# Kernel tuning notes

Hardware: AMD Instinct MI355X
Metric: run time of the kernel (lower is better)

Reference implementation:

```python
import jax, jax.numpy as jnp
import numpy as np

K = 512
U = 2
TEMP_BERN = 0.67
TEMP_CAT = 0.67
EULER = 0.5772156649015329
EPS = 1e-8
UEPS = 1e-6


def setup_inputs() -> dict:
    key = jax.random.key(0)
    ks = jax.random.split(key, 3)
    B, D = 16384, 1024
    inputs = jax.random.normal(ks[0], (B, D), jnp.float32)
    # glorot-normal-ish init for mW
    mW = jax.random.normal(ks[1], (D, K * U), jnp.float32) * jnp.sqrt(2.0 / (D + K * U))
    sW = jnp.full((D, K * U), -5.0, jnp.float32)
    conc1 = jnp.full((K,), 2.0, jnp.float32)
    conc0 = jnp.full((K,), 0.5453, jnp.float32)
    t_pi = jax.random.uniform(ks[2], (D, K), jnp.float32, 4.0, 5.0)
    biases = jnp.full((K * U,), 0.1, jnp.float32)
    return {"inputs": inputs, "mW": mW, "sW": sW, "conc1": conc1,
            "conc0": conc0, "t_pi": t_pi, "biases": biases}


def _uniform(k, shape):
    return jax.random.uniform(k, shape, jnp.float32, UEPS, 1.0 - UEPS)


def reference(inputs, mW, sW, conc1, conc0, t_pi, biases):
    rk = jax.random.split(jax.random.key(42), 4)

    # --- reparameterized weights W = mW + eps * softplus(sW) ---
    sW_sp = jax.nn.softplus(sW)
    eps = jax.lax.stop_gradient(jax.random.normal(rk[0], mW.shape, jnp.float32))
    W = mW + eps * sW_sp
    kl_weights = -0.5 * jnp.mean(2.0 * sW_sp - jnp.square(mW) - jnp.square(sW_sp) + 1.0)
    layer_loss = kl_weights / 60000.0

    # --- IBP: relaxed Bernoulli sample of t_pi ([D, K]) ---
    u = _uniform(rk[1], t_pi.shape)
    logistic = jnp.log(u) - jnp.log1p(-u)
    z_sample = jax.nn.sigmoid((t_pi + logistic) / TEMP_BERN)  # bin_concrete_sample
    z = jnp.tile(z_sample, (1, U))  # [D, K*U], column order u*K+k (as in TF code)

    # Kumaraswamy stick-breaking prior: cumprod along axis 0 (TF default)
    a_sp = jax.nn.softplus(conc1)  # [K]
    b_sp = jax.nn.softplus(conc0)  # [K]
    uk = _uniform(rk[2], t_pi.shape)
    q_u = jnp.power(1.0 - jnp.power(uk, 1.0 / b_sp), 1.0 / a_sp)  # kumaraswamy_sample
    prior_pi = jnp.cumprod(q_u, axis=0)
    q = jax.nn.sigmoid(t_pi)
    kl_z = jnp.sum(q * (jnp.log(q + EPS) - jnp.log(prior_pi + EPS)))

    # KL(Kumaraswamy(a,b) || Beta(1,1)); (beta-1) series term vanishes
    kl_sticks = jnp.sum(((a_sp - 1.0) / a_sp) * (-EULER - jax.scipy.special.digamma(b_sp) - 1.0 / b_sp)
                        + jnp.log(a_sp * b_sp + EPS) - (b_sp - 1.0) / b_sp)
    layer_loss = layer_loss + kl_sticks + kl_z

    W = z * W
    out = inputs @ W + biases  # [B, K*U]

    # --- LWTA activation via Gumbel-softmax over U competitors ---
    logits = out.reshape(-1, K, U)  # [B, K, U]
    g = -jnp.log(-jnp.log(_uniform(rk[3], logits.shape)))
    xi = jax.nn.softmax((logits + g) / TEMP_CAT, axis=-1)  # concrete_sample
    out_act = (logits * xi).reshape(out.shape)
    q_xi = jax.nn.softmax(logits, axis=-1)
    kl_xi = jnp.mean(jnp.sum(q_xi * (jnp.log(q_xi + EPS) - jnp.log(1.0 / U)), axis=1))
    layer_loss = layer_loss + kl_xi

    return out_act, layer_loss
```

## Files before the change

### kernel.cpp

```cpp
#include <hip/hip_runtime.h>
#include <stdint.h>
#include <math.h>

#define B_N   16384
#define D_N   1024
#define K_N   512
#define KU_N  1024
#define EPS_F 1e-8f
#define TEMP  0.67f
#define EULERC 0.5772156649015329f

#define HEPS  524288
#define HU    262144
#define HG    8388608

typedef uint32_t u32;
typedef __attribute__((ext_vector_type(4))) float f32x4;
typedef __attribute__((ext_vector_type(4))) unsigned int u32x4;
typedef __attribute__((ext_vector_type(8))) __bf16 bf16x8;

#define TF_ROT(x, r) (((x) << (r)) | ((x) >> (32 - (r))))

__host__ __device__ static inline void threefry2x32(u32 k0, u32 k1,
                                                    u32 x0, u32 x1,
                                                    u32* o0, u32* o1) {
  u32 ks2 = k0 ^ k1 ^ 0x1BD11BDAu;
  x0 += k0; x1 += k1;
  x0 += x1; x1 = TF_ROT(x1, 13); x1 ^= x0;
  x0 += x1; x1 = TF_ROT(x1, 15); x1 ^= x0;
  x0 += x1; x1 = TF_ROT(x1, 26); x1 ^= x0;
  x0 += x1; x1 = TF_ROT(x1, 6);  x1 ^= x0;
  x0 += k1; x1 += ks2 + 1u;
  x0 += x1; x1 = TF_ROT(x1, 17); x1 ^= x0;
  x0 += x1; x1 = TF_ROT(x1, 29); x1 ^= x0;
  x0 += x1; x1 = TF_ROT(x1, 16); x1 ^= x0;
  x0 += x1; x1 = TF_ROT(x1, 24); x1 ^= x0;
  x0 += ks2; x1 += k0 + 2u;
  x0 += x1; x1 = TF_ROT(x1, 13); x1 ^= x0;
  x0 += x1; x1 = TF_ROT(x1, 15); x1 ^= x0;
  x0 += x1; x1 = TF_ROT(x1, 26); x1 ^= x0;
  x0 += x1; x1 = TF_ROT(x1, 6);  x1 ^= x0;
  x0 += k0; x1 += k1 + 3u;
  x0 += x1; x1 = TF_ROT(x1, 17); x1 ^= x0;
  x0 += x1; x1 = TF_ROT(x1, 29); x1 ^= x0;
  x0 += x1; x1 = TF_ROT(x1, 16); x1 ^= x0;
  x0 += x1; x1 = TF_ROT(x1, 24); x1 ^= x0;
  x0 += k1; x1 += ks2 + 4u;
  x0 += x1; x1 = TF_ROT(x1, 13); x1 ^= x0;
  x0 += x1; x1 = TF_ROT(x1, 15); x1 ^= x0;
  x0 += x1; x1 = TF_ROT(x1, 26); x1 ^= x0;
  x0 += x1; x1 = TF_ROT(x1, 6);  x1 ^= x0;
  x0 += ks2; x1 += k0 + 5u;
  *o0 = x0; *o1 = x1;
}

__device__ static inline float bits_to_u01(u32 b) {
  u32 f = (b >> 9) | 0x3f800000u;
  return __uint_as_float(f) - 1.0f;
}
__device__ static inline float unif_f(u32 b, float lo, float hi) {
  float f = bits_to_u01(b);
  return fmaxf(lo, f * (hi - lo) + lo);
}
__device__ static inline float erfinv_f(float x) {
  float w = -log1pf(-x * x);
  float p;
  if (w < 5.f) {
    w -= 2.5f;
    p = 2.81022636e-08f;
    p = fmaf(p, w, 3.43273939e-07f);
    p = fmaf(p, w, -3.5233877e-06f);
    p = fmaf(p, w, -4.39150654e-06f);
    p = fmaf(p, w, 0.00021858087f);
    p = fmaf(p, w, -0.00125372503f);
    p = fmaf(p, w, -0.00417768164f);
    p = fmaf(p, w, 0.246640727f);
    p = fmaf(p, w, 1.50140941f);
  } else {
    w = sqrtf(w) - 3.f;
    p = -0.000200214257f;
    p = fmaf(p, w, 0.000100950558f);
    p = fmaf(p, w, 0.00134934322f);
    p = fmaf(p, w, -0.00367342844f);
    p = fmaf(p, w, 0.00573950773f);
    p = fmaf(p, w, -0.0076224613f);
    p = fmaf(p, w, 0.00943887047f);
    p = fmaf(p, w, 1.00167406f);
    p = fmaf(p, w, 2.83297682f);
  }
  return p * x;
}
__device__ static inline float softplus_f(float x) {
  return fmaxf(x, 0.f) + log1pf(expf(-fabsf(x)));
}
__device__ static inline float rcp_f(float x) { return __builtin_amdgcn_rcpf(x); }
__device__ static inline float sigmoid_fast(float x) {
  return rcp_f(1.f + __expf(-x));
}
__device__ static inline float digamma_f(float x) {
  float r = 0.f;
  while (x < 6.f) { r -= 1.f / x; x += 1.f; }
  float inv = 1.f / x, inv2 = inv * inv;
  return r + logf(x) - 0.5f * inv
       - inv2 * (1.f / 12.f - inv2 * (1.f / 120.f - inv2 * (1.f / 252.f)));
}
__device__ static inline unsigned short f2bf_rne(float x) {
  u32 u = __float_as_uint(x);
  u32 r = (u + 0x7fffu + ((u >> 16) & 1u)) >> 16;
  return (unsigned short)r;
}
__device__ static inline u32 cvt_pk_bf16(float lo, float hi) {
  u32 r;
  asm("v_cvt_pk_bf16_f32 %0, %1, %2" : "=v"(r) : "v"(lo), "v"(hi));
  return r;
}
__device__ static inline void gload_lds16(const void* g, void* l) {
  __builtin_amdgcn_global_load_lds(
      (const __attribute__((address_space(1))) u32*)g,
      (__attribute__((address_space(3))) u32*)l, 16, 0, 0);
}

__device__ static inline float block_sum(float v) {
  __shared__ float sm[16];
  int lane = threadIdx.x & 63;
  int wid = threadIdx.x >> 6;
  #pragma unroll
  for (int o = 32; o > 0; o >>= 1) v += __shfl_down(v, o, 64);
  if (lane == 0) sm[wid] = v;
  __syncthreads();
  float s = 0.f;
  if (threadIdx.x == 0) {
    int nw = (blockDim.x + 63) >> 6;
    s = sm[0];
    for (int w = 1; w < nw; ++w) s += sm[w];
  }
  return s;
}

__global__ void k_init(const float* __restrict__ conc1,
                       const float* __restrict__ conc0,
                       float* __restrict__ invA, float* __restrict__ invB,
                       float* gacc) {
  int k = threadIdx.x;
  float a = softplus_f(conc1[k]);
  float b = softplus_f(conc0[k]);
  invA[k] = 1.f / a;
  invB[k] = 1.f / b;
  float s = ((a - 1.f) / a) * (-EULERC - digamma_f(b) - 1.f / b)
          + logf(a * b + EPS_F) - (b - 1.f) / b;
  float t = block_sum(s);
  if (threadIdx.x == 0) { gacc[0] = 0.f; gacc[1] = t; gacc[2] = 0.f; }
}

__global__ __launch_bounds__(256) void k_klz_a(const float* __restrict__ invA,
                                               const float* __restrict__ invB,
                                               float* __restrict__ P,
                                               u32 qk0, u32 qk1) {
  int idx = blockIdx.x * 256 + threadIdx.x;
  int c = idx >> 9, k = idx & (K_N - 1);
  float iA = invA[k], iB = invB[k];
  float p = 1.f;
  int d0 = c << 4;
  for (int d = d0; d < d0 + 16; ++d) {
    int n = (d << 9) + k;
    u32 x0 = (n < HU) ? (u32)n : (u32)(n - HU);
    u32 o0, o1;
    threefry2x32(qk0, qk1, x0, x0 + HU, &o0, &o1);
    u32 bits = (n < HU) ? o0 : o1;
    float u = unif_f(bits, 1e-6f, 1.f - 1e-6f);
    p *= powf(1.f - powf(u, iB), iA);
  }
  P[idx] = p;
}

__global__ __launch_bounds__(256) void k_klz_b(const float* __restrict__ t_pi,
                                               const float* __restrict__ invA,
                                               const float* __restrict__ invB,
                                               const float* __restrict__ P,
                                               float* gacc,
                                               u32 qk0, u32 qk1) {
  int idx = blockIdx.x * 256 + threadIdx.x;
  int c = idx >> 9, k = idx & (K_N - 1);
  float iA = invA[k], iB = invB[k];
  float prior = 1.f;
  for (int c2 = 0; c2 < c; ++c2) prior *= P[(c2 << 9) + k];
  float s = 0.f;
  int d0 = c << 4;
  for (int d = d0; d < d0 + 16; ++d) {
    int n = (d << 9) + k;
    u32 x0 = (n < HU) ? (u32)n : (u32)(n - HU);
    u32 o0, o1;
    threefry2x32(qk0, qk1, x0, x0 + HU, &o0, &o1);
    u32 bits = (n < HU) ? o0 : o1;
    float u = unif_f(bits, 1e-6f, 1.f - 1e-6f);
    prior *= powf(1.f - powf(u, iB), iA);
    float q = sigmoid_fast(t_pi[n]);
    s += q * (__logf(q + EPS_F) - __logf(prior + EPS_F));
  }
  float t = block_sum(s);
  if (threadIdx.x == 0) atomicAdd(&gacc[1], t);
}

__global__ __launch_bounds__(256) void k_wbuildT(const float* __restrict__ mW,
                                                 const float* __restrict__ sW,
                                                 const float* __restrict__ t_pi,
                                                 unsigned short* __restrict__ WzT,
                                                 float* __restrict__ gacc,
                                                 u32 ek0, u32 ek1,
                                                 u32 uk0, u32 uk1) {
  __shared__ unsigned short tile[64][65];
  int dt = (int)blockIdx.x >> 4;
  int jt = (int)blockIdx.x & 15;
  int d0 = dt << 6, j0 = jt << 6;
  int tj = threadIdx.x & 63;
  int tr = threadIdx.x >> 6;
  int j = j0 + tj;
  int kk = j & (K_N - 1);
  bool lowD = (dt < 8);
  float klw = 0.f;
  #pragma unroll 4
  for (int rr = 0; rr < 16; ++rr) {
    int dl = (rr << 2) + tr;
    int d = d0 + dl;
    int n = (d << 10) + j;
    u32 x0 = lowD ? (u32)n : (u32)(n - HEPS);
    u32 o0, o1;
    threefry2x32(ek0, ek1, x0, x0 + HEPS, &o0, &o1);
    u32 ebits = lowD ? o0 : o1;
    int nz = (d << 9) + kk;
    u32 zx0 = lowD ? (u32)nz : (u32)(nz - HU);
    u32 z0, z1;
    threefry2x32(uk0, uk1, zx0, zx0 + HU, &z0, &z1);
    u32 zbits = lowD ? z0 : z1;
    float u = unif_f(zbits, 1e-6f, 1.f - 1e-6f);
    float logistic = __logf(u) - log1pf(-u);
    float z = sigmoid_fast((t_pi[nz] + logistic) * (1.f / TEMP));
    float un = unif_f(ebits, -0.99999994f, 1.0f);
    float epsn = 1.41421356f * erfinv_f(un);
    float m = mW[n], sp = softplus_f(sW[n]);
    tile[tj][dl] = f2bf_rne(z * (m + epsn * sp));
    klw += 2.f * sp - m * m - sp * sp + 1.f;
  }
  __syncthreads();
  #pragma unroll 4
  for (int rr = 0; rr < 16; ++rr) {
    int jl = (rr << 2) + tr;
    WzT[(size_t)(j0 + jl) * D_N + d0 + tj] = tile[jl][tj];
  }
  float t = block_sum(klw);
  if (threadIdx.x == 0) atomicAdd(&gacc[0], t);
}

#define GBM 128
#define GBN 128
#define GBK 32

__global__ __launch_bounds__(256) void k_gemm(const float* __restrict__ A,
                                              const unsigned short* __restrict__ Bt,
                                              const float* __restrict__ bias,
                                              float* __restrict__ C) {
  __shared__ __align__(16) unsigned short As[2][GBM * GBK];
  __shared__ __align__(16) unsigned short Bs[2][GBN * GBK];

  int f = (int)blockIdx.x;
  int wk = (f & 7) * 128 + (f >> 3);
  const int brow = (wk >> 3) * GBM;
  const int bcol = (wk & 7) * GBN;

  const int tid = threadIdx.x;
  const int lane = tid & 63;
  const int w = tid >> 6;

  const int ar = tid >> 1;
  const int ac = (tid & 1) << 4;
  const float* gA = A + (size_t)(brow + ar) * D_N + ac;
  const int c0 = (tid & 1) << 1;
  const int aoff0 = (ar << 6) + (((c0    ) ^ (ar & 3)) << 4);
  const int aoff1 = (ar << 6) + (((c0 | 1) ^ (ar & 3)) << 4);

  const int brr = tid >> 2;
  const int bco = ((tid & 3) ^ (brr & 3)) << 3;
  const unsigned short* gB = Bt + (size_t)(bcol + brr) * D_N + bco;
  const int boff0 = (w << 10);
  const int boff1 = 4096 + (w << 10);

  f32x4 acc[4][4];
  #pragma unroll
  for (int m = 0; m < 4; ++m)
    #pragma unroll
    for (int n = 0; n < 4; ++n) acc[m][n] = (f32x4){0.f, 0.f, 0.f, 0.f};

  const int wr = (w >> 1) << 6;
  const int wc = (w & 1) << 6;
  const int fr = lane & 15;
  const int kg = lane >> 4;

  f32x4 a0 = *(const f32x4*)(gA + 0);
  f32x4 a1 = *(const f32x4*)(gA + 4);
  f32x4 a2 = *(const f32x4*)(gA + 8);
  f32x4 a3 = *(const f32x4*)(gA + 12);
  gload_lds16(gB,            (char*)Bs[0] + boff0);
  gload_lds16(gB + 64 * D_N, (char*)Bs[0] + boff1);
  {
    u32x4 p0, p1;
    p0.x = cvt_pk_bf16(a0.x, a0.y); p0.y = cvt_pk_bf16(a0.z, a0.w);
    p0.z = cvt_pk_bf16(a1.x, a1.y); p0.w = cvt_pk_bf16(a1.z, a1.w);
    p1.x = cvt_pk_bf16(a2.x, a2.y); p1.y = cvt_pk_bf16(a2.z, a2.w);
    p1.z = cvt_pk_bf16(a3.x, a3.y); p1.w = cvt_pk_bf16(a3.z, a3.w);
    *(u32x4*)((char*)As[0] + aoff0) = p0;
    *(u32x4*)((char*)As[0] + aoff1) = p1;
  }
  a0 = *(const f32x4*)(gA + GBK + 0);
  a1 = *(const f32x4*)(gA + GBK + 4);
  a2 = *(const f32x4*)(gA + GBK + 8);
  a3 = *(const f32x4*)(gA + GBK + 12);
  __syncthreads();

  #pragma unroll 2
  for (int t = 0; t < 32; ++t) {
    const int cur = t & 1;
    if (t < 31) {
      const int ktn = (t + 1) << 5;
      gload_lds16(gB + ktn,            (char*)Bs[cur ^ 1] + boff0);
      gload_lds16(gB + 64 * D_N + ktn, (char*)Bs[cur ^ 1] + boff1);
      u32x4 p0, p1;
      p0.x = cvt_pk_bf16(a0.x, a0.y); p0.y = cvt_pk_bf16(a0.z, a0.w);
      p0.z = cvt_pk_bf16(a1.x, a1.y); p0.w = cvt_pk_bf16(a1.z, a1.w);
      p1.x = cvt_pk_bf16(a2.x, a2.y); p1.y = cvt_pk_bf16(a2.z, a2.w);
      p1.z = cvt_pk_bf16(a3.x, a3.y); p1.w = cvt_pk_bf16(a3.z, a3.w);
      *(u32x4*)((char*)As[cur ^ 1] + aoff0) = p0;
      *(u32x4*)((char*)As[cur ^ 1] + aoff1) = p1;
      if (t < 30) {
        const float* g = gA + ((t + 2) << 5);
        a0 = *(const f32x4*)(g + 0);
        a1 = *(const f32x4*)(g + 4);
        a2 = *(const f32x4*)(g + 8);
        a3 = *(const f32x4*)(g + 12);
      }
    }
    bf16x8 af[4];
    #pragma unroll
    for (int m = 0; m < 4; ++m) {
      int row = wr + m * 16 + fr;
      af[m] = *(const bf16x8*)((char*)As[cur] + (row << 6) + ((kg ^ (row & 3)) << 4));
    }
    #pragma unroll
    for (int n = 0; n < 4; ++n) {
      int col = wc + n * 16 + fr;
      bf16x8 bf = *(const bf16x8*)((char*)Bs[cur] + (col << 6) + ((kg ^ (col & 3)) << 4));
      #pragma unroll
      for (int m = 0; m < 4; ++m)
        acc[m][n] = __builtin_amdgcn_mfma_f32_16x16x32_bf16(af[m], bf, acc[m][n], 0, 0, 0);
    }
    __syncthreads();
  }

  #pragma unroll
  for (int n = 0; n < 4; ++n) {
    int col = bcol + wc + n * 16 + fr;
    float bv = bias[col];
    #pragma unroll
    for (int m = 0; m < 4; ++m) {
      int rowb = brow + wr + m * 16 + (kg << 2);
      C[(size_t)(rowb + 0) * KU_N + col] = acc[m][n].x + bv;
      C[(size_t)(rowb + 1) * KU_N + col] = acc[m][n].y + bv;
      C[(size_t)(rowb + 2) * KU_N + col] = acc[m][n].z + bv;
      C[(size_t)(rowb + 3) * KU_N + col] = acc[m][n].w + bv;
    }
  }
}

__device__ static inline float lwta_pair(float v0, float v1, u32 ba, u32 bb,
                                         float* o0, float* o1) {
  float u0 = unif_f(ba, 1e-6f, 1.f - 1e-6f);
  float u1 = unif_f(bb, 1e-6f, 1.f - 1e-6f);
  float g0 = -__logf(-__logf(u0));
  float g1 = -__logf(-__logf(u1));
  const float it = 1.f / TEMP;
  float d = ((v1 + g1) - (v0 + g0)) * it;
  float xi0 = rcp_f(1.f + __expf(d));
  float xi1 = 1.f - xi0;
  *o0 = v0 * xi0;
  *o1 = v1 * xi1;
  float qd = v1 - v0;
  float q0 = rcp_f(1.f + __expf(qd));
  float q1 = 1.f - q0;
  const float LOG2F = 0.6931471805599453f;
  return q0 * (__logf(q0 + EPS_F) + LOG2F) + q1 * (__logf(q1 + EPS_F) + LOG2F);
}

__global__ __launch_bounds__(256) void k_epi(float* __restrict__ C,
                                             float* __restrict__ partial,
                                             u32 gk0, u32 gk1) {
  int idx = blockIdx.x * 256 + threadIdx.x;
  int b = idx >> 9;
  int c2 = (idx & 511) << 1;
  size_t p0 = (size_t)b * KU_N + c2;
  size_t p1 = p0 + (size_t)8192 * KU_N;
  float2 r0 = *(const float2*)&C[p0];
  float2 r1 = *(const float2*)&C[p1];
  u32 m = ((u32)b << 10) | (u32)c2;
  u32 x0a, x1a, x0b, x1b;
  threefry2x32(gk0, gk1, m,      m + HG,      &x0a, &x1a);
  threefry2x32(gk0, gk1, m + 1u, m + 1u + HG, &x0b, &x1b);
  float2 w0, w1;
  float kl = lwta_pair(r0.x, r0.y, x0a, x0b, &w0.x, &w0.y)
           + lwta_pair(r1.x, r1.y, x1a, x1b, &w1.x, &w1.y);
  *(float2*)&C[p0] = w0;
  *(float2*)&C[p1] = w1;
  float t = block_sum(kl);
  if (threadIdx.x == 0) partial[blockIdx.x] = t;
}

#define NPART 16384
__global__ __launch_bounds__(256) void k_final(const float* __restrict__ gacc,
                                               const float* __restrict__ partial,
                                               float* __restrict__ out_loss) {
  float s = 0.f;
  for (int i = threadIdx.x; i < NPART; i += 256) s += partial[i];
  float t = block_sum(s);
  if (threadIdx.x == 0) {
    float kl_weights = -0.5f * (gacc[0] * (1.f / 1048576.f));
    out_loss[0] = kl_weights / 60000.f + gacc[1] + t * (1.f / 32768.f);
  }
}

extern "C" void kernel_launch(void* const* d_in, const int* in_sizes, int n_in,
                              void* d_out, int out_size, void* d_ws, size_t ws_size,
                              hipStream_t stream) {
  (void)in_sizes; (void)n_in; (void)out_size; (void)ws_size;
  const float* inputs = (const float*)d_in[0];
  const float* mW     = (const float*)d_in[1];
  const float* sW     = (const float*)d_in[2];
  const float* conc1  = (const float*)d_in[3];
  const float* conc0  = (const float*)d_in[4];
  const float* t_pi   = (const float*)d_in[5];
  const float* biases = (const float*)d_in[6];
  float* out = (float*)d_out;

  u32 a[4], b[4];
  for (int i = 0; i < 4; ++i)
    threefry2x32(0u, 42u, (u32)i, (u32)(i + 4), &a[i], &b[i]);
  u32 e_k0 = a[0], e_k1 = a[1];
  u32 u_k0 = a[2], u_k1 = a[3];
  u32 q_k0 = b[0], q_k1 = b[1];
  u32 g_k0 = b[2], g_k1 = b[3];

  char* wsb = (char*)d_ws;
  unsigned short* WzT = (unsigned short*)wsb;
  float* P       = (float*)(wsb + (2u << 20));
  float* invA    = (float*)(wsb + (2u << 20) + (128u << 10));
  float* invB    = (float*)(wsb + (2u << 20) + (130u << 10));
  float* gacc    = (float*)(wsb + (2u << 20) + (132u << 10));
  float* partial = (float*)(wsb + (2u << 20) + (136u << 10));

  hipLaunchKernelGGL(k_init, dim3(1), dim3(512), 0, stream,
                     conc1, conc0, invA, invB, gacc);
  hipLaunchKernelGGL(k_klz_a, dim3(128), dim3(256), 0, stream,
                     invA, invB, P, q_k0, q_k1);
  hipLaunchKernelGGL(k_klz_b, dim3(128), dim3(256), 0, stream,
                     t_pi, invA, invB, P, gacc, q_k0, q_k1);
  hipLaunchKernelGGL(k_wbuildT, dim3(256), dim3(256), 0, stream,
                     mW, sW, t_pi, WzT, gacc, e_k0, e_k1, u_k0, u_k1);
  hipLaunchKernelGGL(k_gemm, dim3(1024), dim3(256), 0, stream,
                     inputs, WzT, biases, out);
  hipLaunchKernelGGL(k_epi, dim3(NPART), dim3(256), 0, stream,
                     out, partial, g_k0, g_k1);
  hipLaunchKernelGGL(k_final, dim3(1), dim3(256), 0, stream,
                     gacc, partial, out + 16777216);
}
```

Before: 192.7 us.

## Restructure GEMM main loop with explicit waitcnt barrier and peeled last iteration

Rewrites the double-buffered GEMM K-loop so each iteration begins with a manual s_waitcnt (vmcnt(4), lgkmcnt(0)) plus s_barrier instead of ending with __syncthreads. The next B tile's global-to-LDS loads are issued before the MFMA block, and the A conversion and LDS store move after it. The final iteration is peeled out, and sched_barriers pin the instruction order. The goal is to let outstanding A global loads stay in flight across the barrier and to overlap the LDS fills with MFMA work. The hand-written vmcnt count has to match the number of loads actually outstanding, or the kernel can read LDS before it is filled.

```diff
diff --git a/kernel.cpp b/kernel.cpp
--- a/kernel.cpp
+++ b/kernel.cpp
@@ -301,6 +301,7 @@
   f32x4 a3 = *(const f32x4*)(gA + 12);
   gload_lds16(gB,            (char*)Bs[0] + boff0);
   gload_lds16(gB + 64 * D_N, (char*)Bs[0] + boff1);
+  __builtin_amdgcn_sched_barrier(0);
   {
     u32x4 p0, p1;
     p0.x = cvt_pk_bf16(a0.x, a0.y); p0.y = cvt_pk_bf16(a0.z, a0.w);
@@ -314,45 +315,74 @@
   a1 = *(const f32x4*)(gA + GBK + 4);
   a2 = *(const f32x4*)(gA + GBK + 8);
   a3 = *(const f32x4*)(gA + GBK + 12);
-  __syncthreads();
-
-  #pragma unroll 2
-  for (int t = 0; t < 32; ++t) {
+
+  for (int t = 0; t < 31; ++t) {
     const int cur = t & 1;
-    if (t < 31) {
-      const int ktn = (t + 1) << 5;
-      gload_lds16(gB + ktn,            (char*)Bs[cur ^ 1] + boff0);
-      gload_lds16(gB + 64 * D_N + ktn, (char*)Bs[cur ^ 1] + boff1);
+    char* curA = (char*)As + (cur << 13);
+    char* curB = (char*)Bs + (cur << 13);
+    char* altA = (char*)As + ((cur ^ 1) << 13);
+    char* altB = (char*)Bs + ((cur ^ 1) << 13);
+
+    asm volatile("s_waitcnt vmcnt(4) lgkmcnt(0)" ::: "memory");
+    __builtin_amdgcn_s_barrier();
+
+    const int ktn = (t + 1) << 5;
+    gload_lds16(gB + ktn,            altB + boff0);
+    gload_lds16(gB + 64 * D_N + ktn, altB + boff1);
+    __builtin_amdgcn_sched_barrier(0);
+
+    bf16x8 af[4];
+    #pragma unroll
+    for (int m = 0; m < 4; ++m) {
+      int row = wr + m * 16 + fr;
+      af[m] = *(const bf16x8*)(curA + (row << 6) + ((kg ^ (row & 3)) << 4));
+    }
+    #pragma unroll
+    for (int n = 0; n < 4; ++n) {
+      int col = wc + n * 16 + fr;
+      bf16x8 bf = *(const bf16x8*)(curB + (col << 6) + ((kg ^ (col & 3)) << 4));
+      #pragma unroll
+      for (int m = 0; m < 4; ++m)
+        acc[m][n] = __builtin_amdgcn_mfma_f32_16x16x32_bf16(af[m], bf, acc[m][n], 0, 0, 0);
+    }
+
+    {
       u32x4 p0, p1;
       p0.x = cvt_pk_bf16(a0.x, a0.y); p0.y = cvt_pk_bf16(a0.z, a0.w);
       p0.z = cvt_pk_bf16(a1.x, a1.y); p0.w = cvt_pk_bf16(a1.z, a1.w);
       p1.x = cvt_pk_bf16(a2.x, a2.y); p1.y = cvt_pk_bf16(a2.z, a2.w);
       p1.z = cvt_pk_bf16(a3.x, a3.y); p1.w = cvt_pk_bf16(a3.z, a3.w);
-      *(u32x4*)((char*)As[cur ^ 1] + aoff0) = p0;
-      *(u32x4*)((char*)As[cur ^ 1] + aoff1) = p1;
-      if (t < 30) {
-        const float* g = gA + ((t + 2) << 5);
-        a0 = *(const f32x4*)(g + 0);
-        a1 = *(const f32x4*)(g + 4);
-        a2 = *(const f32x4*)(g + 8);
-        a3 = *(const f32x4*)(g + 12);
-      }
-    }
+      *(u32x4*)(altA + aoff0) = p0;
+      *(u32x4*)(altA + aoff1) = p1;
+    }
+    if (t < 30) {
+      const float* g = gA + ((t + 2) << 5);
+      a0 = *(const f32x4*)(g + 0);
+      a1 = *(const f32x4*)(g + 4);
+      a2 = *(const f32x4*)(g + 8);
+      a3 = *(const f32x4*)(g + 12);
+    }
+  }
+
+  asm volatile("s_waitcnt vmcnt(0) lgkmcnt(0)" ::: "memory");
+  __builtin_amdgcn_s_barrier();
+  {
+    char* curA = (char*)As + 8192;
+    char* curB = (char*)Bs + 8192;
     bf16x8 af[4];
     #pragma unroll
     for (int m = 0; m < 4; ++m) {
       int row = wr + m * 16 + fr;
-      af[m] = *(const bf16x8*)((char*)As[cur] + (row << 6) + ((kg ^ (row & 3)) << 4));
+      af[m] = *(const bf16x8*)(curA + (row << 6) + ((kg ^ (row & 3)) << 4));
     }
     #pragma unroll
     for (int n = 0; n < 4; ++n) {
       int col = wc + n * 16 + fr;
-      bf16x8 bf = *(const bf16x8*)((char*)Bs[cur] + (col << 6) + ((kg ^ (col & 3)) << 4));
+      bf16x8 bf = *(const bf16x8*)(curB + (col << 6) + ((kg ^ (col & 3)) << 4));
       #pragma unroll
       for (int m = 0; m < 4; ++m)
         acc[m][n] = __builtin_amdgcn_mfma_f32_16x16x32_bf16(af[m], bf, acc[m][n], 0, 0, 0);
     }
-    __syncthreads();
   }
 
   #pragma unroll
```

After: 188.8 us. 2.0% less time.
